# Performance work log

Measured on AMD Instinct MI355X. Metric: run time of the kernel, lower is better.

## Reference

```python
import jax, jax.numpy as jnp
import numpy as np
import math

T, HW, M, D, DK, H, SIGMA = 16, 1024, 256, 768, 768, 8, 0.5
HD = DK // H
VHD = D // H
EPS = 1e-6
SCALE = 1.0 / math.sqrt(HD)


def _ln(x, g):
    # LayerNorm(eps=1e-6, bias=False)
    m = x.mean(-1, keepdims=True)
    v = ((x - m) ** 2).mean(-1, keepdims=True)
    return (x - m) / jnp.sqrt(v + EPS) * g


def setup_inputs() -> dict:
    key = jax.random.key(0)
    ks = jax.random.split(key, 16)
    s = 0.02
    features = jax.random.normal(ks[0], (T, HW, D), jnp.float32)
    tracks = jax.random.uniform(ks[1], (T, M, 2), jnp.float32)
    track_pos_embeddings = jax.random.normal(ks[2], (T, M, D), jnp.float32)
    feature_pos_embeddings = jax.random.normal(ks[3], (T, HW, D), jnp.float32)
    g = jnp.linspace(0.0, 1.0, 32)
    feature_positions = jnp.stack(jnp.meshgrid(g, g, indexing='ij'), axis=-1).reshape(HW, 2)
    return {
        'features': features,
        'tracks': tracks,
        'feature_positions': feature_positions,
        'track_pos_embeddings': track_pos_embeddings,
        'feature_pos_embeddings': feature_pos_embeddings,
        # AttentionalSampling params (nn.Linear weights are [out,in])
        'Wq_s': jax.random.normal(ks[4], (DK, D)) * s,
        'Wk_s': jax.random.normal(ks[5], (DK, D)) * s,
        'Wv_s': jax.random.normal(ks[6], (D, D)) * s,
        'qg_s': jnp.ones((DK,), jnp.float32),
        'kg_s': jnp.ones((DK,), jnp.float32),
        'Wo_s': jax.random.normal(ks[7], (D, D)) * s,
        # AttentionalSplatting params
        'Wq_p': jax.random.normal(ks[8], (DK, D)) * s,
        'Wk_p': jax.random.normal(ks[9], (DK, D)) * s,
        'Wv_p': jax.random.normal(ks[10], (D, D)) * s,
        'qg_p': jnp.ones((DK,), jnp.float32),
        'kg_p': jnp.ones((DK,), jnp.float32),
        'Wout_p': jax.random.normal(ks[11], (D, D)) * s,
    }


def reference(features, tracks, feature_positions, track_pos_embeddings,
              feature_pos_embeddings, Wq_s, Wk_s, Wv_s, qg_s, kg_s, Wo_s,
              Wq_p, Wk_p, Wv_p, qg_p, kg_p, Wout_p):
    # per-frame Gaussian spatial bias from squared euclidean distances
    # d2[t,m,n] = ||tracks[t,m] - feature_positions[n]||^2  -> [T, M, HW]
    d2 = ((tracks[:, :, None, :] - feature_positions[None, None, :, :]) ** 2).sum(-1)
    bias = -d2 / (2.0 * SIGMA ** 2)  # [T, M, HW]

    # ---- Attentional Sampling: tracks query features ----
    Q = _ln(track_pos_embeddings @ Wq_s.T, qg_s)          # [T, M, DK]
    K = _ln((features + feature_pos_embeddings) @ Wk_s.T, kg_s)  # [T, HW, DK]
    V = features @ Wv_s.T                                  # [T, HW, D]
    Qh = Q.reshape(T, M, H, HD).transpose(0, 2, 1, 3)      # [T, H, M, HD]
    Kh = K.reshape(T, HW, H, HD).transpose(0, 2, 1, 3)     # [T, H, HW, HD]
    Vh = V.reshape(T, HW, H, VHD).transpose(0, 2, 1, 3)    # [T, H, HW, VHD]
    scores = jnp.einsum('thmd,thnd->thmn', Qh, Kh) * SCALE + bias[:, None]
    A = jax.nn.softmax(scores, axis=-1)
    sampled = jnp.einsum('thmn,thnd->thmd', A, Vh)
    sampled = sampled.transpose(0, 2, 1, 3).reshape(T, M, D) @ Wo_s.T  # [T, M, D]

    # ---- Attentional Splatting: features query tracks ----
    Q2 = _ln(feature_pos_embeddings @ Wq_p.T, qg_p)        # [T, HW, DK]
    K2 = _ln(track_pos_embeddings @ Wk_p.T, kg_p)          # [T, M, DK]
    V2 = sampled @ Wv_p.T                                   # [T, M, D]
    Q2h = Q2.reshape(T, HW, H, HD).transpose(0, 2, 1, 3)   # [T, H, HW, HD]
    K2h = K2.reshape(T, M, H, HD).transpose(0, 2, 1, 3)    # [T, H, M, HD]
    V2h = V2.reshape(T, M, H, VHD).transpose(0, 2, 1, 3)   # [T, H, M, VHD]
    bias_t = jnp.swapaxes(bias, 1, 2)                       # [T, HW, M] (cdist is symmetric)
    scores2 = jnp.einsum('thnd,thmd->thnm', Q2h, K2h) * SCALE + bias_t[:, None]
    A2 = jax.nn.softmax(scores2, axis=-1)
    upd = jnp.einsum('thnm,thmd->thnd', A2, V2h)
    feature_updates = upd.transpose(0, 2, 1, 3).reshape(T, HW, D) @ Wout_p.T
    return features + feature_updates
```

## Files before the change

### kernel.cpp

```cpp
#include <hip/hip_runtime.h>

#define DD 768
#define HDIM 96
#define ATT_SCALE 0.10206207261596575f

typedef float floatx4 __attribute__((ext_vector_type(4)));
typedef __bf16 bf16;
typedef bf16 bf16x8 __attribute__((ext_vector_type(8)));
typedef bf16 bf16x4 __attribute__((ext_vector_type(4)));
typedef bf16 bf16x2 __attribute__((ext_vector_type(2)));

__device__ __forceinline__ void gl2lds16(const bf16* g, bf16* l) {
  __builtin_amdgcn_global_load_lds(
      (const __attribute__((address_space(1))) void*)g,
      (__attribute__((address_space(3))) void*)l, 16, 0, 0);
}

__global__ __launch_bounds__(256) void conv_fuse(const float* __restrict__ f,
                                                 const float* __restrict__ e,
                                                 bf16* __restrict__ fb,
                                                 bf16* __restrict__ xb,
                                                 bf16* __restrict__ eb) {
  const int i = (blockIdx.x * 256 + threadIdx.x) * 8;
  floatx4 f0 = *(const floatx4*)(f + i);
  floatx4 f1 = *(const floatx4*)(f + i + 4);
  floatx4 e0 = *(const floatx4*)(e + i);
  floatx4 e1 = *(const floatx4*)(e + i + 4);
  bf16x8 fv, xv, ev;
#pragma unroll
  for (int k = 0; k < 4; k++) {
    fv[k] = (bf16)f0[k];           fv[k + 4] = (bf16)f1[k];
    ev[k] = (bf16)e0[k];           ev[k + 4] = (bf16)e1[k];
    xv[k] = (bf16)(f0[k] + e0[k]); xv[k + 4] = (bf16)(f1[k] + e1[k]);
  }
  *(bf16x8*)(fb + i) = fv;
  *(bf16x8*)(xb + i) = xv;
  *(bf16x8*)(eb + i) = ev;
}

__global__ __launch_bounds__(256) void f2b(const float* __restrict__ s,
                                           bf16* __restrict__ d) {
  const int i = (blockIdx.x * 256 + threadIdx.x) * 8;
  floatx4 s0 = *(const floatx4*)(s + i);
  floatx4 s1 = *(const floatx4*)(s + i + 4);
  bf16x8 v;
#pragma unroll
  for (int k = 0; k < 4; k++) { v[k] = (bf16)s0[k]; v[k + 4] = (bf16)s1[k]; }
  *(bf16x8*)(d + i) = v;
}

__global__ __launch_bounds__(256) void wconv(const float* w0, const float* w1,
                                             const float* w2, const float* w3,
                                             const float* w4, const float* w5,
                                             const float* w6, const float* w7,
                                             bf16* __restrict__ dst) {
  const float* srcs[8] = {w0, w1, w2, w3, w4, w5, w6, w7};
  const float* s = srcs[blockIdx.y];
  bf16* d = dst + (size_t)blockIdx.y * 589824;
  const int i = (blockIdx.x * 256 + threadIdx.x) * 8;
  floatx4 s0 = *(const floatx4*)(s + i);
  floatx4 s1 = *(const floatx4*)(s + i + 4);
  bf16x8 v;
#pragma unroll
  for (int k = 0; k < 4; k++) { v[k] = (bf16)s0[k]; v[k + 4] = (bf16)s1[k]; }
  *(bf16x8*)(d + i) = v;
}

__global__ __launch_bounds__(256) void wtrans(const float* __restrict__ in,
                                              bf16* __restrict__ out) {
  __shared__ float Ts[64][65];
  const int X0 = blockIdx.x * 64, Y0 = blockIdx.y * 64;
  const int r = threadIdx.x >> 2;
  const int c4 = (threadIdx.x & 3) * 16;
  const float* src = in + (size_t)(Y0 + r) * DD + X0 + c4;
#pragma unroll
  for (int k = 0; k < 16; k += 4) {
    floatx4 v = *(const floatx4*)(src + k);
    Ts[r][c4 + k] = v[0]; Ts[r][c4 + k + 1] = v[1];
    Ts[r][c4 + k + 2] = v[2]; Ts[r][c4 + k + 3] = v[3];
  }
  __syncthreads();
  bf16 o[16];
#pragma unroll
  for (int k = 0; k < 16; k++) o[k] = (bf16)Ts[c4 + k][r];
  *(bf16x8*)(out + (size_t)(X0 + r) * DD + Y0 + c4) = *(bf16x8*)&o[0];
  *(bf16x8*)(out + (size_t)(X0 + r) * DD + Y0 + c4 + 8) = *(bf16x8*)&o[8];
}

__device__ __forceinline__ void ln_row(bf16* x, const float* g, int lane) {
  float v[12], s = 0.f, ss = 0.f;
#pragma unroll
  for (int j = 0; j < 3; j++) {
    bf16x4 b = *(const bf16x4*)&x[j * 256 + lane * 4];
#pragma unroll
    for (int e = 0; e < 4; e++) {
      float t = (float)b[e];
      v[j * 4 + e] = t; s += t; ss += t * t;
    }
  }
#pragma unroll
  for (int o = 32; o > 0; o >>= 1) { s += __shfl_xor(s, o); ss += __shfl_xor(ss, o); }
  const float mean = s * (1.0f / DD);
  const float inv = rsqrtf(ss * (1.0f / DD) - mean * mean + 1e-6f);
#pragma unroll
  for (int j = 0; j < 3; j++) {
    floatx4 gg = *(const floatx4*)&g[j * 256 + lane * 4];
    bf16x4 o4;
#pragma unroll
    for (int e = 0; e < 4; e++) o4[e] = (bf16)((v[j * 4 + e] - mean) * inv * gg[e]);
    *(bf16x4*)&x[j * 256 + lane * 4] = o4;
  }
}

__global__ __launch_bounds__(256) void ln_all(bf16* X0, const float* g0,
                                              bf16* X1, const float* g1,
                                              bf16* X2, const float* g2,
                                              bf16* X3, const float* g3) {
  const int b = blockIdx.x;
  bf16* X; const float* g; int base;
  if (b < 4096)      { X = X0; g = g0; base = b; }
  else if (b < 8192) { X = X1; g = g1; base = b - 4096; }
  else if (b < 9216) { X = X2; g = g2; base = b - 8192; }
  else               { X = X3; g = g3; base = b - 9216; }
  const int w = threadIdx.x >> 6, lane = threadIdx.x & 63;
  ln_row(X + (size_t)(base * 4 + w) * DD, g, lane);
}

template <int MODE>
__device__ __forceinline__ void gemm_core(const bf16* __restrict__ A,
                                          const bf16* __restrict__ W,
                                          bf16* __restrict__ Cb,
                                          float* __restrict__ Cf,
                                          const float* __restrict__ addsrc,
                                          bf16* As, bf16* Ws) {
  const int tid = threadIdx.x;
  const int lane = tid & 63;
  const int w = tid >> 6;
  const int row0 = blockIdx.x * 128;
  const int col0 = blockIdx.y * 128;
  const int wm = (w & 1) * 64;
  const int wn = (w >> 1) * 64;
  const int fr = lane & 15;
  const int quad = lane >> 4;
  const int srow = tid >> 2;
  const int scol = (tid & 3) * 8;
  const bf16* Ag = A + (size_t)(row0 + srow) * DD + scol;
  const bf16* Wg = W + (size_t)(col0 + srow) * DD + scol;
  bf16* AsD = &As[tid * 8];
  bf16* WsD = &Ws[tid * 8];

  floatx4 acc[4][4];
#pragma unroll
  for (int i = 0; i < 4; i++)
#pragma unroll
    for (int j = 0; j < 4; j++) acc[i][j] = (floatx4){0, 0, 0, 0};

  for (int k0 = 0; k0 < DD; k0 += 32) {
    __syncthreads();
    gl2lds16(Ag + k0, AsD);
    gl2lds16(Ag + k0 + (size_t)64 * DD, AsD + 2048);
    gl2lds16(Wg + k0, WsD);
    gl2lds16(Wg + k0 + (size_t)64 * DD, WsD + 2048);
    __syncthreads();
    bf16x8 af[4], bfr[4];
#pragma unroll
    for (int i = 0; i < 4; i++)
      af[i] = *(const bf16x8*)&As[(wm + i * 16 + fr) * 32 + quad * 8];
#pragma unroll
    for (int j = 0; j < 4; j++)
      bfr[j] = *(const bf16x8*)&Ws[(wn + j * 16 + fr) * 32 + quad * 8];
#pragma unroll
    for (int i = 0; i < 4; i++)
#pragma unroll
      for (int j = 0; j < 4; j++)
        acc[i][j] = __builtin_amdgcn_mfma_f32_16x16x32_bf16(af[i], bfr[j], acc[i][j], 0, 0, 0);
  }
#pragma unroll
  for (int i = 0; i < 4; i++)
#pragma unroll
    for (int j = 0; j < 4; j++)
#pragma unroll
      for (int r = 0; r < 4; r++) {
        const int row = row0 + wm + i * 16 + quad * 4 + r;
        const int col = col0 + wn + j * 16 + fr;
        const size_t idx = (size_t)row * DD + col;
        if (MODE == 0) Cb[idx] = (bf16)acc[i][j][r];
        else Cf[idx] = acc[i][j][r] + addsrc[idx];
      }
}

__global__ __launch_bounds__(256) void gemm_b(const bf16* A, const bf16* W, bf16* C) {
  __shared__ bf16 As[4096], Ws[4096];
  gemm_core<0>(A, W, C, nullptr, nullptr, As, Ws);
}

__global__ __launch_bounds__(256) void gemm_b2(const bf16* A0, const bf16* W0, bf16* C0,
                                               const bf16* A1, const bf16* W1, bf16* C1) {
  __shared__ bf16 As[4096], Ws[4096];
  if (blockIdx.z == 0) gemm_core<0>(A0, W0, C0, nullptr, nullptr, As, Ws);
  else                 gemm_core<0>(A1, W1, C1, nullptr, nullptr, As, Ws);
}

__global__ __launch_bounds__(256) void gemm_b3(const bf16* A0, const bf16* W0, bf16* C0,
                                               const bf16* A1, const bf16* W1, bf16* C1,
                                               const bf16* A2, const bf16* W2, bf16* C2) {
  __shared__ bf16 As[4096], Ws[4096];
  if (blockIdx.z == 0)      gemm_core<0>(A0, W0, C0, nullptr, nullptr, As, Ws);
  else if (blockIdx.z == 1) gemm_core<0>(A1, W1, C1, nullptr, nullptr, As, Ws);
  else                      gemm_core<0>(A2, W2, C2, nullptr, nullptr, As, Ws);
}

__global__ __launch_bounds__(256) void gemm_final(const bf16* A, const bf16* W,
                                                  float* C, const float* addsrc) {
  __shared__ bf16 As[4096], Ws[4096];
  gemm_core<1>(A, W, nullptr, C, addsrc, As, Ws);
}

template <int SPLIT>
__global__ __launch_bounds__(512, 4) void attn512(
    const bf16* __restrict__ Qb, const bf16* __restrict__ Kb,
    const bf16* __restrict__ Vb, bf16* __restrict__ Ob,
    float* __restrict__ Ml,
    const float* __restrict__ qpos, int qpos_ts,
    const float* __restrict__ kpos, int kpos_ts,
    int nq, int nk, int npq, int nsp) {
  const int b = blockIdx.x;
  const int h = b & 7;
  const int t = (b >> 3) & 15;
  const int rest = b >> 7;
  const int qt = rest % npq;
  const int sp = rest / npq;
  const int klen = nk / nsp;
  const int k0s = sp * klen;
  const int q0 = qt * 128;
  const bf16* Q = Qb + (size_t)t * nq * DD + h * HDIM;
  const bf16* K = Kb + (size_t)t * nk * DD + h * HDIM;
  const bf16* V = Vb + (size_t)t * nk * DD + h * HDIM;
  bf16* O = Ob + (size_t)(SPLIT ? (sp * 16 + t) : t) * nq * DD + h * HDIM;
  const float* qp = qpos + (size_t)t * qpos_ts;
  const float* kp = kpos + (size_t)t * kpos_ts;

  __shared__ bf16 Ks[64 * 104];
  __shared__ bf16 Vt[96 * 72];
  __shared__ bf16 Ps[2 * 64 * 72];

  const int tid = threadIdx.x;
  const int w = tid >> 6;
  const int g = w >> 2;
  const int wl = w & 3;
  const int lane = tid & 63;
  const int fr = lane & 15;
  const int quad = lane >> 4;
  const int rowb = wl * 16;
  const int qgb = q0 + g * 64;
  bf16* Pg = &Ps[g * 64 * 72];

  bf16x8 qf[3];
  {
    const bf16* qrow = Q + (size_t)(qgb + rowb + fr) * DD;
#pragma unroll
    for (int c = 0; c < 3; c++) qf[c] = *(const bf16x8*)(qrow + c * 32 + quad * 8);
  }
  float qx[4], qy[4];
#pragma unroll
  for (int r = 0; r < 4; r++) {
    int qi = qgb + rowb + quad * 4 + r;
    qx[r] = qp[qi * 2];
    qy[r] = qp[qi * 2 + 1];
  }

  float lrow[4] = {0.f, 0.f, 0.f, 0.f};
  floatx4 oacc[6];
#pragma unroll
  for (int d = 0; d < 6; d++) oacc[d] = (floatx4){0, 0, 0, 0};

  const int krA = tid >> 3, kcA = (tid & 7) * 8;
  const int krB = (tid & 255) >> 2, kcB = 64 + (tid & 3) * 8;
  const int nb = (tid & 31) * 2, db = (tid >> 5) * 6;

  for (int n0 = k0s; n0 < k0s + klen; n0 += 64) {
    __syncthreads();
    *(bf16x8*)&Ks[krA * 104 + kcA] =
        *(const bf16x8*)(K + (size_t)(n0 + krA) * DD + kcA);
    if (tid < 256)
      *(bf16x8*)&Ks[krB * 104 + kcB] =
          *(const bf16x8*)(K + (size_t)(n0 + krB) * DD + kcB);
    {
      bf16 tmp[2][6];
#pragma unroll
      for (int nn = 0; nn < 2; nn++) {
        const unsigned* vg = (const unsigned*)(V + (size_t)(n0 + nb + nn) * DD + db);
        unsigned u0 = vg[0], u1 = vg[1], u2 = vg[2];
        *(unsigned*)&tmp[nn][0] = u0;
        *(unsigned*)&tmp[nn][2] = u1;
        *(unsigned*)&tmp[nn][4] = u2;
      }
#pragma unroll
      for (int dd = 0; dd < 6; dd++) {
        bf16x2 v2 = {tmp[0][dd], tmp[1][dd]};
        *(bf16x2*)&Vt[(db + dd) * 72 + nb] = v2;
      }
    }
    __syncthreads();

    floatx4 s4[4];
#pragma unroll
    for (int j = 0; j < 4; j++) {
      floatx4 sa = {0, 0, 0, 0};
#pragma unroll
      for (int c = 0; c < 3; c++) {
        bf16x8 kf = *(const bf16x8*)&Ks[(j * 16 + fr) * 104 + c * 32 + quad * 8];
        sa = __builtin_amdgcn_mfma_f32_16x16x32_bf16(qf[c], kf, sa, 0, 0, 0);
      }
      s4[j] = sa;
    }
    float kxx[4], kyy[4];
#pragma unroll
    for (int j = 0; j < 4; j++) {
      int ki = (n0 + j * 16 + fr) * 2;
      kxx[j] = kp[ki];
      kyy[j] = kp[ki + 1];
    }
#pragma unroll
    for (int j = 0; j < 4; j++)
#pragma unroll
      for (int r = 0; r < 4; r++) {
        float dx = qx[r] - kxx[j], dy = qy[r] - kyy[j];
        float sv = s4[j][r] * ATT_SCALE - 2.0f * (dx * dx + dy * dy);
        float pv = __expf(sv);
        lrow[r] += pv;
        Pg[(rowb + quad * 4 + r) * 72 + j * 16 + fr] = (bf16)pv;
      }
    bf16x8 pf0 = *(const bf16x8*)&Pg[(rowb + fr) * 72 + quad * 8];
    bf16x8 pf1 = *(const bf16x8*)&Pg[(rowb + fr) * 72 + 32 + quad * 8];
#pragma unroll
    for (int d = 0; d < 6; d++) {
      bf16x8 v0 = *(const bf16x8*)&Vt[(d * 16 + fr) * 72 + quad * 8];
      bf16x8 v1 = *(const bf16x8*)&Vt[(d * 16 + fr) * 72 + 32 + quad * 8];
      oacc[d] = __builtin_amdgcn_mfma_f32_16x16x32_bf16(pf0, v0, oacc[d], 0, 0, 0);
      oacc[d] = __builtin_amdgcn_mfma_f32_16x16x32_bf16(pf1, v1, oacc[d], 0, 0, 0);
    }
  }

#pragma unroll
  for (int r = 0; r < 4; r++)
#pragma unroll
    for (int o = 1; o < 16; o <<= 1) lrow[r] += __shfl_xor(lrow[r], o);

#pragma unroll
  for (int r = 0; r < 4; r++) {
    int row = qgb + rowb + quad * 4 + r;
    if (SPLIT) {
#pragma unroll
      for (int d = 0; d < 6; d++)
        O[(size_t)row * DD + d * 16 + fr] = (bf16)oacc[d][r];
      if (fr == 0)
        Ml[((size_t)(sp * 16 + t) * 8 + h) * nq + row] = lrow[r];
    } else {
      float inv = 1.0f / lrow[r];
#pragma unroll
      for (int d = 0; d < 6; d++)
        O[(size_t)row * DD + d * 16 + fr] = (bf16)(oacc[d][r] * inv);
    }
  }
}

__global__ __launch_bounds__(256) void combine4(const bf16* __restrict__ Op,
                                                const float* __restrict__ Ml,
                                                bf16* __restrict__ Out) {
  const int row = blockIdx.x;
  const int t = row >> 8;
  const int q = row & 255;
#pragma unroll
  for (int e = 0; e < 3; e++) {
    int dim = threadIdx.x + e * 256;
    int hh = dim / 96;
    float osum = 0.f, lsum = 0.f;
#pragma unroll
    for (int s = 0; s < 4; s++) {
      lsum += Ml[((size_t)(s * 16 + t) * 8 + hh) * 256 + q];
      osum += (float)Op[((size_t)(s * 16 + t) * 256 + q) * DD + dim];
    }
    Out[(size_t)row * DD + dim] = (bf16)(osum / lsum);
  }
}

extern "C" void kernel_launch(void* const* d_in, const int* in_sizes, int n_in,
                              void* d_out, int out_size, void* d_ws, size_t ws_size,
                              hipStream_t stream) {
  const float* features = (const float*)d_in[0];
  const float* tracks   = (const float*)d_in[1];
  const float* fpos     = (const float*)d_in[2];
  const float* tpe      = (const float*)d_in[3];
  const float* fpe      = (const float*)d_in[4];
  const float* Wq_s     = (const float*)d_in[5];
  const float* Wk_s     = (const float*)d_in[6];
  const float* Wv_s     = (const float*)d_in[7];
  const float* qg_s     = (const float*)d_in[8];
  const float* kg_s     = (const float*)d_in[9];
  const float* Wo_s     = (const float*)d_in[10];
  const float* Wq_p     = (const float*)d_in[11];
  const float* Wk_p     = (const float*)d_in[12];
  const float* Wv_p     = (const float*)d_in[13];
  const float* qg_p     = (const float*)d_in[14];
  const float* kg_p     = (const float*)d_in[15];
  const float* Wout_p   = (const float*)d_in[16];
  float* out = (float*)d_out;

  const size_t SB = (size_t)16 * 1024 * 768;
  const size_t SS = (size_t)16 * 256 * 768;
  const size_t SW = (size_t)768 * 768;
  bf16* p = (bf16*)d_ws;
  bf16* Fb  = p; p += SB;
  bf16* Xb  = p; p += SB;
  bf16* Feb = p; p += SB;
  bf16* Kc  = p; p += SB;
  bf16* Vc  = p; p += SB;
  bf16* Qb2 = p; p += SB;
  bf16* Tb  = p; p += SS;
  bf16* Qc  = p; p += SS;
  bf16* K2  = p; p += SS;
  bf16* Sh  = p; p += SS;
  bf16* Op  = p; p += 4 * SS;
  bf16* Wb  = p; p += 8 * SW;
  bf16* WoT = p; p += SW;
  bf16* Wcr = p; p += SW;
  float* Ml = (float*)p;
  bf16* V2 = Qc; bf16* U = Fb;

  dim3 blk(256);

  conv_fuse<<<6144, blk, 0, stream>>>(features, fpe, Fb, Xb, Feb);
  f2b<<<1536, blk, 0, stream>>>(tpe, Tb);
  wconv<<<dim3(288, 8), blk, 0, stream>>>(Wq_s, Wk_s, Wv_s, Wo_s,
                                          Wq_p, Wk_p, Wv_p, Wout_p, Wb);
  wtrans<<<dim3(12, 12), blk, 0, stream>>>(Wo_s, WoT);
  gemm_b<<<dim3(6, 6), blk, 0, stream>>>(Wb + 6 * SW, WoT, Wcr);
  gemm_b3<<<dim3(128, 6, 3), blk, 0, stream>>>(Xb, Wb + 1 * SW, Kc,
                                               Fb, Wb + 2 * SW, Vc,
                                               Feb, Wb + 4 * SW, Qb2);
  gemm_b2<<<dim3(32, 6, 2), blk, 0, stream>>>(Tb, Wb + 0 * SW, Qc,
                                              Tb, Wb + 5 * SW, K2);
  ln_all<<<10240, blk, 0, stream>>>(Kc, kg_s, Qb2, qg_p, Qc, qg_s, K2, kg_p);
  attn512<1><<<1024, dim3(512), 0, stream>>>(Qc, Kc, Vc, Op, Ml,
                                             tracks, 512, fpos, 0, 256, 1024, 2, 4);
  combine4<<<4096, blk, 0, stream>>>(Op, Ml, Sh);
  gemm_b<<<dim3(32, 6), blk, 0, stream>>>(Sh, Wcr, V2);
  attn512<0><<<1024, dim3(512), 0, stream>>>(Qb2, K2, V2, U, nullptr,
                                             fpos, 0, tracks, 512, 1024, 256, 8, 1);
  gemm_final<<<dim3(128, 6), blk, 0, stream>>>(U, Wb + 7 * SW, out, features);
}
```

Measured before the change: 491.4 us.

## Merge prep kernels into one launch and batch projection GEMMs with K=64 steps

Folds the four conversion/transpose kernels into a single prep kernel dispatched by block index. The three earlier GEMM launches become one gemm_all grid, which also absorbs the small Wcr weight product. The GEMM core now loads a 64-wide K slice per sync, halving the number of barrier rounds at the cost of double the LDS footprint. The intent is to cut launch overhead and inter-kernel gaps and to reduce sync stalls. The larger LDS may lower occupancy, and many gemm_all blocks in z=3 (x>=70) do nothing.

```diff
diff --git a/kernel.cpp b/kernel.cpp
--- a/kernel.cpp
+++ b/kernel.cpp
@@ -16,75 +16,72 @@
       (__attribute__((address_space(3))) void*)l, 16, 0, 0);
 }
 
-__global__ __launch_bounds__(256) void conv_fuse(const float* __restrict__ f,
-                                                 const float* __restrict__ e,
-                                                 bf16* __restrict__ fb,
-                                                 bf16* __restrict__ xb,
-                                                 bf16* __restrict__ eb) {
-  const int i = (blockIdx.x * 256 + threadIdx.x) * 8;
-  floatx4 f0 = *(const floatx4*)(f + i);
-  floatx4 f1 = *(const floatx4*)(f + i + 4);
-  floatx4 e0 = *(const floatx4*)(e + i);
-  floatx4 e1 = *(const floatx4*)(e + i + 4);
-  bf16x8 fv, xv, ev;
-#pragma unroll
-  for (int k = 0; k < 4; k++) {
-    fv[k] = (bf16)f0[k];           fv[k + 4] = (bf16)f1[k];
-    ev[k] = (bf16)e0[k];           ev[k + 4] = (bf16)e1[k];
-    xv[k] = (bf16)(f0[k] + e0[k]); xv[k + 4] = (bf16)(f1[k] + e1[k]);
-  }
-  *(bf16x8*)(fb + i) = fv;
-  *(bf16x8*)(xb + i) = xv;
-  *(bf16x8*)(eb + i) = ev;
-}
-
-__global__ __launch_bounds__(256) void f2b(const float* __restrict__ s,
-                                           bf16* __restrict__ d) {
-  const int i = (blockIdx.x * 256 + threadIdx.x) * 8;
-  floatx4 s0 = *(const floatx4*)(s + i);
-  floatx4 s1 = *(const floatx4*)(s + i + 4);
-  bf16x8 v;
-#pragma unroll
-  for (int k = 0; k < 4; k++) { v[k] = (bf16)s0[k]; v[k + 4] = (bf16)s1[k]; }
-  *(bf16x8*)(d + i) = v;
-}
-
-__global__ __launch_bounds__(256) void wconv(const float* w0, const float* w1,
-                                             const float* w2, const float* w3,
-                                             const float* w4, const float* w5,
-                                             const float* w6, const float* w7,
-                                             bf16* __restrict__ dst) {
-  const float* srcs[8] = {w0, w1, w2, w3, w4, w5, w6, w7};
-  const float* s = srcs[blockIdx.y];
-  bf16* d = dst + (size_t)blockIdx.y * 589824;
-  const int i = (blockIdx.x * 256 + threadIdx.x) * 8;
-  floatx4 s0 = *(const floatx4*)(s + i);
-  floatx4 s1 = *(const floatx4*)(s + i + 4);
-  bf16x8 v;
-#pragma unroll
-  for (int k = 0; k < 4; k++) { v[k] = (bf16)s0[k]; v[k + 4] = (bf16)s1[k]; }
-  *(bf16x8*)(d + i) = v;
-}
-
-__global__ __launch_bounds__(256) void wtrans(const float* __restrict__ in,
-                                              bf16* __restrict__ out) {
-  __shared__ float Ts[64][65];
-  const int X0 = blockIdx.x * 64, Y0 = blockIdx.y * 64;
-  const int r = threadIdx.x >> 2;
-  const int c4 = (threadIdx.x & 3) * 16;
-  const float* src = in + (size_t)(Y0 + r) * DD + X0 + c4;
-#pragma unroll
-  for (int k = 0; k < 16; k += 4) {
-    floatx4 v = *(const floatx4*)(src + k);
-    Ts[r][c4 + k] = v[0]; Ts[r][c4 + k + 1] = v[1];
-    Ts[r][c4 + k + 2] = v[2]; Ts[r][c4 + k + 3] = v[3];
-  }
-  __syncthreads();
-  bf16 o[16];
-#pragma unroll
-  for (int k = 0; k < 16; k++) o[k] = (bf16)Ts[c4 + k][r];
-  *(bf16x8*)(out + (size_t)(X0 + r) * DD + Y0 + c4) = *(bf16x8*)&o[0];
-  *(bf16x8*)(out + (size_t)(X0 + r) * DD + Y0 + c4 + 8) = *(bf16x8*)&o[8];
+__global__ __launch_bounds__(256) void prep(
+    const float* __restrict__ features, const float* __restrict__ fpe,
+    const float* __restrict__ tpe,
+    const float* w0, const float* w1, const float* w2, const float* w3,
+    const float* w4, const float* w5, const float* w6, const float* w7,
+    bf16* __restrict__ Fb, bf16* __restrict__ Xb, bf16* __restrict__ Feb,
+    bf16* __restrict__ Tb, bf16* __restrict__ Wb, bf16* __restrict__ WoT) {
+  const int b = blockIdx.x;
+  const int tid = threadIdx.x;
+  if (b < 6144) {
+    const int i = (b * 256 + tid) * 8;
+    floatx4 f0 = *(const floatx4*)(features + i);
+    floatx4 f1 = *(const floatx4*)(features + i + 4);
+    floatx4 e0 = *(const floatx4*)(fpe + i);
+    floatx4 e1 = *(const floatx4*)(fpe + i + 4);
+    bf16x8 fv, xv, ev;
+#pragma unroll
+    for (int k = 0; k < 4; k++) {
+      fv[k] = (bf16)f0[k];           fv[k + 4] = (bf16)f1[k];
+      ev[k] = (bf16)e0[k];           ev[k + 4] = (bf16)e1[k];
+      xv[k] = (bf16)(f0[k] + e0[k]); xv[k + 4] = (bf16)(f1[k] + e1[k]);
+    }
+    *(bf16x8*)(Fb + i) = fv;
+    *(bf16x8*)(Xb + i) = xv;
+    *(bf16x8*)(Feb + i) = ev;
+  } else if (b < 7680) {
+    const int i = ((b - 6144) * 256 + tid) * 8;
+    floatx4 s0 = *(const floatx4*)(tpe + i);
+    floatx4 s1 = *(const floatx4*)(tpe + i + 4);
+    bf16x8 v;
+#pragma unroll
+    for (int k = 0; k < 4; k++) { v[k] = (bf16)s0[k]; v[k + 4] = (bf16)s1[k]; }
+    *(bf16x8*)(Tb + i) = v;
+  } else if (b < 9984) {
+    const int sub = b - 7680;
+    const int wi = sub / 288, xb = sub % 288;
+    const float* srcs[8] = {w0, w1, w2, w3, w4, w5, w6, w7};
+    const float* s = srcs[wi];
+    bf16* d = Wb + (size_t)wi * 589824;
+    const int i = (xb * 256 + tid) * 8;
+    floatx4 s0 = *(const floatx4*)(s + i);
+    floatx4 s1 = *(const floatx4*)(s + i + 4);
+    bf16x8 v;
+#pragma unroll
+    for (int k = 0; k < 4; k++) { v[k] = (bf16)s0[k]; v[k + 4] = (bf16)s1[k]; }
+    *(bf16x8*)(d + i) = v;
+  } else {
+    __shared__ float Ts[64][65];
+    const int sub = b - 9984;
+    const int X0 = (sub % 12) * 64, Y0 = (sub / 12) * 64;
+    const int r = tid >> 2;
+    const int c4 = (tid & 3) * 16;
+    const float* src = w3 + (size_t)(Y0 + r) * DD + X0 + c4;
+#pragma unroll
+    for (int k = 0; k < 16; k += 4) {
+      floatx4 v = *(const floatx4*)(src + k);
+      Ts[r][c4 + k] = v[0]; Ts[r][c4 + k + 1] = v[1];
+      Ts[r][c4 + k + 2] = v[2]; Ts[r][c4 + k + 3] = v[3];
+    }
+    __syncthreads();
+    bf16 o[16];
+#pragma unroll
+    for (int k = 0; k < 16; k++) o[k] = (bf16)Ts[c4 + k][r];
+    *(bf16x8*)(WoT + (size_t)(X0 + r) * DD + Y0 + c4) = *(bf16x8*)&o[0];
+    *(bf16x8*)(WoT + (size_t)(X0 + r) * DD + Y0 + c4 + 8) = *(bf16x8*)&o[8];
+  }
 }
 
 __device__ __forceinline__ void ln_row(bf16* x, const float* g, int lane) {
@@ -127,17 +124,16 @@
 }
 
 template <int MODE>
-__device__ __forceinline__ void gemm_core(const bf16* __restrict__ A,
-                                          const bf16* __restrict__ W,
-                                          bf16* __restrict__ Cb,
-                                          float* __restrict__ Cf,
-                                          const float* __restrict__ addsrc,
-                                          bf16* As, bf16* Ws) {
+__device__ __forceinline__ void gemm_core64(const bf16* __restrict__ A,
+                                            const bf16* __restrict__ W,
+                                            bf16* __restrict__ Cb,
+                                            float* __restrict__ Cf,
+                                            const float* __restrict__ addsrc,
+                                            bf16* As, bf16* Ws,
+                                            int row0, int col0) {
   const int tid = threadIdx.x;
   const int lane = tid & 63;
   const int w = tid >> 6;
-  const int row0 = blockIdx.x * 128;
-  const int col0 = blockIdx.y * 128;
   const int wm = (w & 1) * 64;
   const int wn = (w >> 1) * 64;
   const int fr = lane & 15;
@@ -155,25 +151,34 @@
 #pragma unroll
     for (int j = 0; j < 4; j++) acc[i][j] = (floatx4){0, 0, 0, 0};
 
-  for (int k0 = 0; k0 < DD; k0 += 32) {
+  for (int k0 = 0; k0 < DD; k0 += 64) {
     __syncthreads();
     gl2lds16(Ag + k0, AsD);
     gl2lds16(Ag + k0 + (size_t)64 * DD, AsD + 2048);
     gl2lds16(Wg + k0, WsD);
     gl2lds16(Wg + k0 + (size_t)64 * DD, WsD + 2048);
+    gl2lds16(Ag + k0 + 32, AsD + 4096);
+    gl2lds16(Ag + k0 + 32 + (size_t)64 * DD, AsD + 4096 + 2048);
+    gl2lds16(Wg + k0 + 32, WsD + 4096);
+    gl2lds16(Wg + k0 + 32 + (size_t)64 * DD, WsD + 4096 + 2048);
     __syncthreads();
-    bf16x8 af[4], bfr[4];
-#pragma unroll
-    for (int i = 0; i < 4; i++)
-      af[i] = *(const bf16x8*)&As[(wm + i * 16 + fr) * 32 + quad * 8];
-#pragma unroll
-    for (int j = 0; j < 4; j++)
-      bfr[j] = *(const bf16x8*)&Ws[(wn + j * 16 + fr) * 32 + quad * 8];
-#pragma unroll
-    for (int i = 0; i < 4; i++)
+#pragma unroll
+    for (int half = 0; half < 2; half++) {
+      const bf16* Ah = As + half * 4096;
+      const bf16* Wh = Ws + half * 4096;
+      bf16x8 af[4], bfr[4];
+#pragma unroll
+      for (int i = 0; i < 4; i++)
+        af[i] = *(const bf16x8*)&Ah[(wm + i * 16 + fr) * 32 + quad * 8];
 #pragma unroll
       for (int j = 0; j < 4; j++)
-        acc[i][j] = __builtin_amdgcn_mfma_f32_16x16x32_bf16(af[i], bfr[j], acc[i][j], 0, 0, 0);
+        bfr[j] = *(const bf16x8*)&Wh[(wn + j * 16 + fr) * 32 + quad * 8];
+#pragma unroll
+      for (int i = 0; i < 4; i++)
+#pragma unroll
+        for (int j = 0; j < 4; j++)
+          acc[i][j] = __builtin_amdgcn_mfma_f32_16x16x32_bf16(af[i], bfr[j], acc[i][j], 0, 0, 0);
+    }
   }
 #pragma unroll
   for (int i = 0; i < 4; i++)
@@ -189,31 +194,45 @@
       }
 }
 
+__global__ __launch_bounds__(256) void gemm_all(
+    const bf16* Xb, const bf16* Fb, const bf16* Feb, const bf16* Tb,
+    const bf16* Wb, const bf16* WoT,
+    bf16* Kc, bf16* Vc, bf16* Qb2, bf16* Qc, bf16* K2, bf16* Wcr) {
+  __shared__ bf16 As[8192], Ws[8192];
+  const size_t SW = (size_t)768 * 768;
+  const int z = blockIdx.z;
+  if (z == 0)
+    gemm_core64<0>(Xb, Wb + 1 * SW, Kc, nullptr, nullptr, As, Ws,
+                   blockIdx.x * 128, blockIdx.y * 128);
+  else if (z == 1)
+    gemm_core64<0>(Fb, Wb + 2 * SW, Vc, nullptr, nullptr, As, Ws,
+                   blockIdx.x * 128, blockIdx.y * 128);
+  else if (z == 2)
+    gemm_core64<0>(Feb, Wb + 4 * SW, Qb2, nullptr, nullptr, As, Ws,
+                   blockIdx.x * 128, blockIdx.y * 128);
+  else {
+    const int x = blockIdx.x;
+    if (x < 32)
+      gemm_core64<0>(Tb, Wb + 0 * SW, Qc, nullptr, nullptr, As, Ws,
+                     x * 128, blockIdx.y * 128);
+    else if (x < 64)
+      gemm_core64<0>(Tb, Wb + 5 * SW, K2, nullptr, nullptr, As, Ws,
+                     (x - 32) * 128, blockIdx.y * 128);
+    else if (x < 70)
+      gemm_core64<0>(Wb + 6 * SW, WoT, Wcr, nullptr, nullptr, As, Ws,
+                     (x - 64) * 128, blockIdx.y * 128);
+  }
+}
+
 __global__ __launch_bounds__(256) void gemm_b(const bf16* A, const bf16* W, bf16* C) {
-  __shared__ bf16 As[4096], Ws[4096];
-  gemm_core<0>(A, W, C, nullptr, nullptr, As, Ws);
-}
-
-__global__ __launch_bounds__(256) void gemm_b2(const bf16* A0, const bf16* W0, bf16* C0,
-                                               const bf16* A1, const bf16* W1, bf16* C1) {
-  __shared__ bf16 As[4096], Ws[4096];
-  if (blockIdx.z == 0) gemm_core<0>(A0, W0, C0, nullptr, nullptr, As, Ws);
-  else                 gemm_core<0>(A1, W1, C1, nullptr, nullptr, As, Ws);
-}
-
-__global__ __launch_bounds__(256) void gemm_b3(const bf16* A0, const bf16* W0, bf16* C0,
-                                               const bf16* A1, const bf16* W1, bf16* C1,
-                                               const bf16* A2, const bf16* W2, bf16* C2) {
-  __shared__ bf16 As[4096], Ws[4096];
-  if (blockIdx.z == 0)      gemm_core<0>(A0, W0, C0, nullptr, nullptr, As, Ws);
-  else if (blockIdx.z == 1) gemm_core<0>(A1, W1, C1, nullptr, nullptr, As, Ws);
-  else                      gemm_core<0>(A2, W2, C2, nullptr, nullptr, As, Ws);
+  __shared__ bf16 As[8192], Ws[8192];
+  gemm_core64<0>(A, W, C, nullptr, nullptr, As, Ws, blockIdx.x * 128, blockIdx.y * 128);
 }
 
 __global__ __launch_bounds__(256) void gemm_final(const bf16* A, const bf16* W,
                                                   float* C, const float* addsrc) {
-  __shared__ bf16 As[4096], Ws[4096];
-  gemm_core<1>(A, W, nullptr, C, addsrc, As, Ws);
+  __shared__ bf16 As[8192], Ws[8192];
+  gemm_core64<1>(A, W, nullptr, C, addsrc, As, Ws, blockIdx.x * 128, blockIdx.y * 128);
 }
 
 template <int SPLIT>
@@ -430,17 +449,11 @@
 
   dim3 blk(256);
 
-  conv_fuse<<<6144, blk, 0, stream>>>(features, fpe, Fb, Xb, Feb);
-  f2b<<<1536, blk, 0, stream>>>(tpe, Tb);
-  wconv<<<dim3(288, 8), blk, 0, stream>>>(Wq_s, Wk_s, Wv_s, Wo_s,
-                                          Wq_p, Wk_p, Wv_p, Wout_p, Wb);
-  wtrans<<<dim3(12, 12), blk, 0, stream>>>(Wo_s, WoT);
-  gemm_b<<<dim3(6, 6), blk, 0, stream>>>(Wb + 6 * SW, WoT, Wcr);
-  gemm_b3<<<dim3(128, 6, 3), blk, 0, stream>>>(Xb, Wb + 1 * SW, Kc,
-                                               Fb, Wb + 2 * SW, Vc,
-                                               Feb, Wb + 4 * SW, Qb2);
-  gemm_b2<<<dim3(32, 6, 2), blk, 0, stream>>>(Tb, Wb + 0 * SW, Qc,
-                                              Tb, Wb + 5 * SW, K2);
+  prep<<<10128, blk, 0, stream>>>(features, fpe, tpe,
+                                  Wq_s, Wk_s, Wv_s, Wo_s, Wq_p, Wk_p, Wv_p, Wout_p,
+                                  Fb, Xb, Feb, Tb, Wb, WoT);
+  gemm_all<<<dim3(128, 6, 4), blk, 0, stream>>>(Xb, Fb, Feb, Tb, Wb, WoT,
+                                                Kc, Vc, Qb2, Qc, K2, Wcr);
   ln_all<<<10240, blk, 0, stream>>>(Kc, kg_s, Qb2, qg_p, Qc, qg_s, K2, kg_p);
   attn512<1><<<1024, dim3(512), 0, stream>>>(Qc, Kc, Vc, Op, Ml,
                                              tracks, 512, fpos, 0, 256, 1024, 2, 4);
```

Measured after the change: 475.2 us. -3.3%, faster.
